# Performance work log

Measured on AMD Instinct MI355X. Metric: run time of the kernel, lower is better.

## Reference

```python
import jax, jax.numpy as jnp
import numpy as np

N_TOKENS = 2048
HIDDEN = 1024
INTER = 2816
N_EXPERTS = 8
N_ADAPTERS = 2
MAX_RANK = 16
TOP_K = 2
N_SEQS = 8


def setup_inputs() -> dict:
    key = jax.random.key(0)
    ks = jax.random.split(key, 12)
    f32 = jnp.float32
    std = 0.02
    hidden_states = jax.random.normal(ks[0], (N_TOKENS, HIDDEN), f32)
    topk_ids = jax.random.randint(ks[1], (N_TOKENS, TOP_K), 0, N_EXPERTS)
    tw = jax.random.uniform(ks[2], (N_TOKENS, TOP_K), dtype=f32)
    topk_weights = tw / tw.sum(axis=-1, keepdims=True)
    gate_a = jax.random.normal(ks[3], (N_ADAPTERS, N_EXPERTS, MAX_RANK, HIDDEN), f32) * std
    gate_b = jax.random.normal(ks[4], (N_ADAPTERS, N_EXPERTS, INTER, MAX_RANK), f32) * std
    up_a = jax.random.normal(ks[5], (N_ADAPTERS, N_EXPERTS, MAX_RANK, HIDDEN), f32) * std
    up_b = jax.random.normal(ks[6], (N_ADAPTERS, N_EXPERTS, INTER, MAX_RANK), f32) * std
    down_a = jax.random.normal(ks[7], (N_ADAPTERS, N_EXPERTS, MAX_RANK, INTER), f32) * std
    down_b = jax.random.normal(ks[8], (N_ADAPTERS, N_EXPERTS, HIDDEN, MAX_RANK), f32) * std
    weight_indices = jax.random.randint(ks[9], (N_SEQS,), 0, N_ADAPTERS)
    seq_lens = jnp.full((N_SEQS,), N_TOKENS // N_SEQS, dtype=jnp.int32)
    lora_ranks = jnp.array([16, 8], dtype=jnp.int32)
    scalings = jnp.array([2.0, 1.0], dtype=f32)
    base_gate_up_weight = jax.random.normal(ks[10], (N_EXPERTS, 2 * INTER, HIDDEN), f32) * std
    base_down_weight = jax.random.normal(ks[11], (N_EXPERTS, HIDDEN, INTER), f32) * std
    return {
        'hidden_states': hidden_states, 'topk_ids': topk_ids, 'topk_weights': topk_weights,
        'gate_a': gate_a, 'gate_b': gate_b, 'up_a': up_a, 'up_b': up_b,
        'down_a': down_a, 'down_b': down_b, 'weight_indices': weight_indices,
        'seq_lens': seq_lens, 'lora_ranks': lora_ranks, 'scalings': scalings,
        'base_gate_up_weight': base_gate_up_weight, 'base_down_weight': base_down_weight,
    }


def _forward(hidden_states, topk_ids, topk_weights, gate_a, gate_b, up_a, up_b,
             down_a, down_b, weight_indices, seq_lens, lora_ranks, scalings,
             base_gate_up_weight, base_down_weight):
    N, H = hidden_states.shape
    A, E, R, _ = gate_a.shape
    I = gate_b.shape[2]
    x = hidden_states.astype(jnp.float32)
    # token -> sequence -> adapter (replaces the per-token python loop)
    token_to_seq = jnp.searchsorted(jnp.cumsum(seq_lens), jnp.arange(N), side='right')
    adapter = weight_indices[token_to_seq]                               # [N]
    scale_t = scalings[adapter].astype(jnp.float32)[:, None]             # [N,1]
    # per-adapter rank truncation A[:rank] == zeroing rows r >= rank of LoRA-A
    rmask = (jnp.arange(R)[None, :] < lora_ranks[:, None]).astype(jnp.float32)  # [A,R]
    ga = gate_a.astype(jnp.float32) * rmask[:, None, :, None]
    ua = up_a.astype(jnp.float32) * rmask[:, None, :, None]
    da = down_a.astype(jnp.float32) * rmask[:, None, :, None]
    gb = gate_b.astype(jnp.float32)
    ub = up_b.astype(jnp.float32)
    db = down_b.astype(jnp.float32)
    # low-rank input projections for all adapters & experts (tiny: N*A*E*R)
    z_gate = jnp.einsum('nh,aerh->naer', x, ga)
    z_up = jnp.einsum('nh,aerh->naer', x, ua)
    sel = adapter[:, None, None]
    Wgu = base_gate_up_weight.astype(jnp.float32)   # [E, 2I, H]
    Wd = base_down_weight.astype(jnp.float32)       # [E, H, I]
    out = jnp.zeros((N, H), jnp.float32)
    for e in range(E):
        # summed routing weight for this expert per token (0 => no contribution)
        w_e = jnp.where(topk_ids == e, topk_weights, 0.0).sum(axis=1).astype(jnp.float32)  # [N]
        base_gate = x @ Wgu[e, :I].T                 # [N,I]
        base_up = x @ Wgu[e, I:].T                   # [N,I]
        lg = jnp.take_along_axis(jnp.einsum('nar,air->nai', z_gate[:, :, e], gb[:, e]), sel, axis=1)[:, 0]
        lu = jnp.take_along_axis(jnp.einsum('nar,air->nai', z_up[:, :, e], ub[:, e]), sel, axis=1)[:, 0]
        gate_out = base_gate + scale_t * lg
        up_out = base_up + scale_t * lu
        act = jax.nn.silu(gate_out) * up_out         # [N,I]
        zd = jnp.einsum('ni,ari->nar', act, da[:, e])
        ld = jnp.take_along_axis(jnp.einsum('nar,ahr->nah', zd, db[:, e]), sel, axis=1)[:, 0]
        base_down = act @ Wd[e].T                    # [N,H]
        out = out + w_e[:, None] * (base_down + scale_t * ld)
    return out.astype(hidden_states.dtype)


def reference(hidden_states, topk_ids, topk_weights, gate_a, gate_b, up_a, up_b,
              down_a, down_b, weight_indices, seq_lens, lora_ranks, scalings,
              base_gate_up_weight, base_down_weight):
    return _forward(hidden_states, topk_ids, topk_weights, gate_a, gate_b, up_a, up_b,
                    down_a, down_b, weight_indices, seq_lens, lora_ranks, scalings,
                    base_gate_up_weight, base_down_weight)
```

## Files before the change

### kernel.cpp

```cpp
#include <hip/hip_runtime.h>
#include <hip/hip_bf16.h>
#include <math.h>

#define N_TOK   2048
#define HIDDEN  1024
#define INTER   2816
#define NEXP    8
#define NADAPT  2
#define MAXRANK 16
#define TOPK    2
#define NSEQ    8
#define NPAIRS  (N_TOK*TOPK)
#define NGU     (2*INTER)

typedef unsigned short u16;
typedef __attribute__((ext_vector_type(8))) short bf16x8;
typedef __attribute__((ext_vector_type(4))) float f32x4;

#define F_CNT   0u
#define F_PERM  4096u
#define F_ZG    139264u
#define F_ZU    401408u
#define F_ZD    663552u
#define F_XBF   1048576u
#define F_ACT   5242880u
#define F_GB    28311552u
#define F_UB    29753344u
#define F_DB    31195136u
#define F_GA_BF 31719424u
#define F_UA_BF 32243712u
#define F_ZDF   32768000u
#define F_WGU   33554432u
#define F_WD    125829120u
#define F_DA_BF F_XBF
#define FAST_NEED 171966464u

#define B_CNT   0u
#define B_PERM  4096u
#define B_ZG    262144u
#define B_ZU    524288u
#define B_ZD    786432u
#define B_ACT   1048576u

__device__ __forceinline__ float bf2f(u16 u){
  union { unsigned int i; float f; } v; v.i = ((unsigned int)u)<<16; return v.f;
}
__device__ __forceinline__ u16 f2bf(float f){
  union { float f; unsigned int i; } v; v.f = f;
  unsigned int i = v.i;
  return (u16)((i + 0x7fffu + ((i>>16)&1u)) >> 16);
}
__device__ __forceinline__ uint4 cvt8(const float* src){
  float4 lo = *(const float4*)src;
  float4 hi = *(const float4*)(src+4);
  uint4 r;
  r.x = (unsigned)f2bf(lo.x) | ((unsigned)f2bf(lo.y)<<16);
  r.y = (unsigned)f2bf(lo.z) | ((unsigned)f2bf(lo.w)<<16);
  r.z = (unsigned)f2bf(hi.x) | ((unsigned)f2bf(hi.y)<<16);
  r.w = (unsigned)f2bf(hi.z) | ((unsigned)f2bf(hi.w)<<16);
  return r;
}
__device__ __forceinline__ uint2 cvt4(float4 v){
  uint2 r;
  r.x = (unsigned)f2bf(v.x) | ((unsigned)f2bf(v.y)<<16);
  r.y = (unsigned)f2bf(v.z) | ((unsigned)f2bf(v.w)<<16);
  return r;
}

__device__ __forceinline__ void gl16(const void* g, void* l){
  __builtin_amdgcn_global_load_lds(
      (const __attribute__((address_space(1))) unsigned int*)g,
      (__attribute__((address_space(3))) unsigned int*)l, 16, 0, 0);
}

__device__ __forceinline__ int token_adapter(int n, const int* seq_lens, const int* widx){
  int cum = 0;
  #pragma unroll
  for (int s = 0; s < NSEQ; ++s){ cum += seq_lens[s]; if (n < cum) return widx[s]; }
  return widx[NSEQ-1];
}

__global__ void k_zero(float* outf, int* cnt, float* zdf){
  int t = threadIdx.x;
  if (blockIdx.x < 2048){
    int id = blockIdx.x*256 + t;
    *(float4*)&outf[(size_t)id*4] = make_float4(0.f,0.f,0.f,0.f);
  } else {
    int id = (blockIdx.x - 2048)*256 + t;
    *(float4*)&zdf[(size_t)id*4] = make_float4(0.f,0.f,0.f,0.f);
  }
  if (blockIdx.x == 0 && t < NEXP) cnt[t] = 0;
}

__global__ void k_route(const int* __restrict__ topk_ids, int* cnt, int* perm){
  int p = blockIdx.x*256 + threadIdx.x;
  if (p >= NPAIRS) return;
  int e = topk_ids[p];
  int pos = atomicAdd(&cnt[e], 1);
  perm[e*NPAIRS + pos] = p;
}

__global__ void k_cvt(const float* __restrict__ src, u16* __restrict__ dst, int n4){
  int id = blockIdx.x*256 + threadIdx.x;
  if (id >= n4) return;
  ((uint2*)dst)[id] = cvt4(((const float4*)src)[id]);
}

__global__ void k_cvt_all(
    const float* __restrict__ x,  const float* __restrict__ wgu, const float* __restrict__ wd,
    const float* __restrict__ gb, const float* __restrict__ ub,  const float* __restrict__ db_,
    const float* __restrict__ ga, const float* __restrict__ ua,
    u16* xb, u16* wgub, u16* wdb, u16* gbb, u16* ubb, u16* dbb, u16* gab, u16* uab,
    float* outf, float* zdf, int* cnt)
{
  int b = blockIdx.x;
  int t = threadIdx.x;
  if (b == 0 && t < NEXP) cnt[t] = 0;
  if (b >= 35904){
    float* dz; size_t i4;
    if (b < 37952){ dz = outf; i4 = (size_t)(b - 35904)*256 + t; }
    else          { dz = zdf;  i4 = (size_t)(b - 37952)*256 + t; }
    ((float4*)dz)[i4] = make_float4(0.f,0.f,0.f,0.f);
    return;
  }
  const float* src; u16* dst; int base;
  if      (b < 1024)  { src = x;   dst = xb;   base = 0; }
  else if (b < 23552) { src = wgu; dst = wgub; base = 1024; }
  else if (b < 34816) { src = wd;  dst = wdb;  base = 23552; }
  else if (b < 35168) { src = gb;  dst = gbb;  base = 34816; }
  else if (b < 35520) { src = ub;  dst = ubb;  base = 35168; }
  else if (b < 35648) { src = db_; dst = dbb;  base = 35520; }
  else if (b < 35776) { src = ga;  dst = gab;  base = 35648; }
  else                { src = ua;  dst = uab;  base = 35776; }
  size_t i4 = (size_t)(b - base)*512 + t;
  float4 v0 = ((const float4*)src)[i4];
  float4 v1 = ((const float4*)src)[i4 + 256];
  ((uint2*)dst)[i4]       = cvt4(v0);
  ((uint2*)dst)[i4 + 256] = cvt4(v1);
}

__global__ __launch_bounds__(256) void k_zgu_mfma(
    const u16* __restrict__ xb, const u16* __restrict__ gab, const u16* __restrict__ uab,
    const int* __restrict__ cnt, const int* __restrict__ perm,
    const int* __restrict__ widx, const int* __restrict__ seq_lens,
    const int* __restrict__ ranks, const float* __restrict__ scal,
    u16* __restrict__ zg, u16* __restrict__ zu)
{
  int e = blockIdx.y;
  int me = cnt[e];
  int tm = blockIdx.x;
  if (tm*64 >= me) return;
  int t = threadIdx.x;

  __shared__ __align__(16) u16 As[64*32];
  __shared__ __align__(16) u16 Bs[64*32];

  int r0 = t >> 2;
  int kc = ((t&3) - r0) & 3;
  int ko = kc*8;
  int mg = tm*64 + r0;
  int pa = perm[e*NPAIRS + min(mg, me-1)];
  const u16* arow = xb + (size_t)(pa>>1)*HIDDEN + ko;
  int jr = r0 & 31;
  const u16* brow = (r0 < 32 ? gab : uab)
                    + (size_t)(((jr>>4)*NEXP + e)*MAXRANK + (jr&15))*HIDDEN + ko;

  int wv = t>>6, lane = t&63;
  u16* Asw = &As[wv*512];
  u16* Bsw = &Bs[wv*512];
  int wm = wv>>1, wn = wv&1;
  int l15 = lane&15, q = lane>>4;

  f32x4 acc[2][2] = {};
  int aoff[2], boff[2];
  #pragma unroll
  for (int i=0;i<2;++i){ int row = wm*32 + i*16 + l15; aoff[i] = row*32 + ((q+row)&3)*8; }
  #pragma unroll
  for (int j=0;j<2;++j){ int row = wn*32 + j*16 + l15; boff[j] = row*32 + ((q+row)&3)*8; }

  for (int kt = 0; kt < HIDDEN/32; ++kt){
    __syncthreads();
    gl16(arow + kt*32, Asw);
    gl16(brow + kt*32, Bsw);
    __syncthreads();
    bf16x8 af[2], bfr[2];
    #pragma unroll
    for (int i=0;i<2;++i) af[i] = *(const bf16x8*)&As[aoff[i]];
    #pragma unroll
    for (int j=0;j<2;++j) bfr[j] = *(const bf16x8*)&Bs[boff[j]];
    #pragma unroll
    for (int i=0;i<2;++i)
      #pragma unroll
      for (int j=0;j<2;++j)
        acc[i][j] = __builtin_amdgcn_mfma_f32_16x16x32_bf16(af[i], bfr[j], acc[i][j],0,0,0);
  }

  u16* dstz = wn ? zu : zg;
  #pragma unroll
  for (int i=0;i<2;++i){
    #pragma unroll
    for (int r=0;r<4;++r){
      int mgo = tm*64 + wm*32 + i*16 + q*4 + r;
      if (mgo < me){
        int p = perm[e*NPAIRS + mgo];
        int a = token_adapter(p>>1, seq_lens, widx);
        int rank = ranks[a]; float sc = scal[a];
        #pragma unroll
        for (int j=0;j<2;++j){
          int jc = j*16 + l15;
          float v = ((jc>>4)==a && (jc&15)<rank) ? sc*acc[i][j][r] : 0.f;
          dstz[(size_t)p*32 + jc] = f2bf(v);
        }
      }
    }
  }
}

__global__ __launch_bounds__(256) void k_zd_mfma(
    const u16* __restrict__ act, const u16* __restrict__ dab,
    const int* __restrict__ cnt, const int* __restrict__ perm,
    const int* __restrict__ widx, const int* __restrict__ seq_lens,
    const int* __restrict__ ranks, const float* __restrict__ scal,
    float* __restrict__ zdf)
{
  int e = blockIdx.z;
  int me = cnt[e];
  int tm = blockIdx.y;
  if (tm*64 >= me) return;
  int ks = blockIdx.x;
  int t = threadIdx.x;

  __shared__ __align__(16) u16 As[64*32];
  __shared__ __align__(16) u16 Bs[32*32];

  int r0 = t >> 2;
  int kc = ((t&3) - r0) & 3;
  int ko = kc*8;
  int mg = tm*64 + r0;
  int pa = perm[e*NPAIRS + min(mg, me-1)];
  const u16* arow = act + (size_t)pa*INTER + ko;
  int jr = r0 & 31;
  const u16* brow = dab + (size_t)(((jr>>4)*NEXP + e)*MAXRANK + (jr&15))*INTER + ko;

  int wv = t>>6, lane = t&63;
  u16* Asw = &As[wv*512];
  u16* Bsw = &Bs[(wv&1)*512];
  int l15 = lane&15, q = lane>>4;

  f32x4 acc[2] = {};
  int aoff; { int row = wv*16 + l15; aoff = row*32 + ((q+row)&3)*8; }
  int boff[2];
  #pragma unroll
  for (int j=0;j<2;++j){ int row = j*16 + l15; boff[j] = row*32 + ((q+row)&3)*8; }

  int kt0 = ks*22, kt1 = kt0 + 22;
  for (int kt = kt0; kt < kt1; ++kt){
    __syncthreads();
    gl16(arow + kt*32, Asw);
    if (wv < 2) gl16(brow + kt*32, Bsw);
    __syncthreads();
    bf16x8 af = *(const bf16x8*)&As[aoff];
    bf16x8 b0 = *(const bf16x8*)&Bs[boff[0]];
    bf16x8 b1 = *(const bf16x8*)&Bs[boff[1]];
    acc[0] = __builtin_amdgcn_mfma_f32_16x16x32_bf16(af, b0, acc[0],0,0,0);
    acc[1] = __builtin_amdgcn_mfma_f32_16x16x32_bf16(af, b1, acc[1],0,0,0);
  }

  #pragma unroll
  for (int r=0;r<4;++r){
    int mgo = tm*64 + wv*16 + q*4 + r;
    if (mgo < me){
      int p = perm[e*NPAIRS + mgo];
      int a = token_adapter(p>>1, seq_lens, widx);
      int rank = ranks[a]; float sc = scal[a];
      #pragma unroll
      for (int j=0;j<2;++j){
        int jc = j*16 + l15;
        if ((jc>>4)==a && (jc&15)<rank)
          atomicAdd(&zdf[(size_t)p*32 + jc], sc*acc[j][r]);
      }
    }
  }
}

__global__ __launch_bounds__(256) void k_zgu(
    const float* __restrict__ x, const int* __restrict__ topk_ids,
    const float* __restrict__ gate_a, const float* __restrict__ up_a,
    const int* __restrict__ widx, const int* __restrict__ seq_lens,
    const int* __restrict__ ranks, const float* __restrict__ scal,
    u16* __restrict__ zg, u16* __restrict__ zu)
{
  int p = blockIdx.x, n = p >> 1, t = threadIdx.x;
  int e = topk_ids[p];
  __shared__ float xs[HIDDEN];
  for (int i = t; i < HIDDEN; i += 256) xs[i] = x[(size_t)n*HIDDEN + i];
  if (t < 32){ zg[p*32 + t] = 0; zu[p*32 + t] = 0; }
  __syncthreads();
  int a = token_adapter(n, seq_lens, widx);
  int rank = ranks[a];
  float scale = scal[a];
  int wv = t >> 6, lane = t & 63;
  for (int i = 0; i < 8; ++i){
    int o = wv*8 + i;
    int r = o & 15;
    const float* wrow = ((o < 16) ? gate_a : up_a) + (size_t)((a*NEXP + e)*MAXRANK + r)*HIDDEN;
    float s = 0.f;
    for (int h = lane; h < HIDDEN; h += 64) s += xs[h] * wrow[h];
    s += __shfl_down(s,32); s += __shfl_down(s,16); s += __shfl_down(s,8);
    s += __shfl_down(s,4);  s += __shfl_down(s,2);  s += __shfl_down(s,1);
    if (lane == 0 && r < rank)
      (o < 16 ? zg : zu)[p*32 + a*16 + r] = f2bf(scale * s);
  }
}

__global__ __launch_bounds__(256) void k_zd(
    const u16* __restrict__ act, const int* __restrict__ topk_ids,
    const float* __restrict__ down_a,
    const int* __restrict__ widx, const int* __restrict__ seq_lens,
    const int* __restrict__ ranks, const float* __restrict__ scal,
    u16* __restrict__ zd)
{
  int p = blockIdx.x, n = p >> 1, t = threadIdx.x;
  int e = topk_ids[p];
  __shared__ float as_[INTER];
  for (int i = t; i < INTER; i += 256) as_[i] = bf2f(act[(size_t)p*INTER + i]);
  if (t < 32) zd[p*32 + t] = 0;
  __syncthreads();
  int a = token_adapter(n, seq_lens, widx);
  int rank = ranks[a];
  float scale = scal[a];
  int wv = t >> 6, lane = t & 63;
  for (int i = 0; i < 4; ++i){
    int r = wv*4 + i;
    const float* wrow = down_a + (size_t)((a*NEXP + e)*MAXRANK + r)*INTER;
    float s = 0.f;
    for (int h = lane; h < INTER; h += 64) s += as_[h] * wrow[h];
    s += __shfl_down(s,32); s += __shfl_down(s,16); s += __shfl_down(s,8);
    s += __shfl_down(s,4);  s += __shfl_down(s,2);  s += __shfl_down(s,1);
    if (lane == 0 && r < rank) zd[p*32 + a*16 + r] = f2bf(scale * s);
  }
}

__global__ __launch_bounds__(256) void k_gufused_bf(
    const u16* __restrict__ xb, const u16* __restrict__ wgu,
    const u16* __restrict__ gbb, const u16* __restrict__ ubb,
    const u16* __restrict__ zg, const u16* __restrict__ zu,
    const int* __restrict__ cnt, const int* __restrict__ perm,
    u16* __restrict__ act)
{
  int e = blockIdx.z;
  int me = cnt[e];
  int tm = blockIdx.y;
  if (tm*128 >= me) return;
  int tn = blockIdx.x;
  int t = threadIdx.x;

  __shared__ __align__(16) u16 As[128*32];
  __shared__ __align__(16) u16 Bg[64*32];
  __shared__ __align__(16) u16 Bu[64*32];

  int r0 = t >> 2;
  int kc = ((t&3) - r0) & 3;
  int ko = kc*8;
  int mg0 = tm*128 + r0, mg1 = mg0 + 64;
  int p0 = perm[e*NPAIRS + min(mg0, me-1)];
  int p1 = perm[e*NPAIRS + min(mg1, me-1)];
  const u16* arow0 = xb + (size_t)(p0>>1)*HIDDEN + ko;
  const u16* arow1 = xb + (size_t)(p1>>1)*HIDDEN + ko;
  int jg = tn*64 + r0;
  const u16* browg = wgu + ((size_t)e*NGU + jg)*HIDDEN + ko;
  const u16* browu = wgu + ((size_t)e*NGU + INTER + jg)*HIDDEN + ko;

  int wvb = (t>>6)*512;
  u16* Asw0 = &As[wvb];
  u16* Asw1 = &As[2048 + wvb];
  u16* Bgw  = &Bg[wvb];
  u16* Buw  = &Bu[wvb];

  int wv = t>>6, lane = t&63;
  int wm = wv>>1, wn = wv&1;
  int l15 = lane&15, q = lane>>4;

  f32x4 accg[4][2] = {};
  f32x4 accu[4][2] = {};
  int aoff[4], boff[2];
  #pragma unroll
  for (int i=0;i<4;++i){ int row = wm*64 + i*16 + l15; aoff[i] = row*32 + ((q+row)&3)*8; }
  #pragma unroll
  for (int j=0;j<2;++j){ int row = wn*32 + j*16 + l15; boff[j] = row*32 + ((q+row)&3)*8; }

  for (int kt = 0; kt < HIDDEN/32; ++kt){
    __syncthreads();
    gl16(arow0 + kt*32, Asw0);
    gl16(arow1 + kt*32, Asw1);
    gl16(browg + kt*32, Bgw);
    gl16(browu + kt*32, Buw);
    __syncthreads();
    bf16x8 af[4], bgf[2], buf[2];
    #pragma unroll
    for (int i=0;i<4;++i) af[i] = *(const bf16x8*)&As[aoff[i]];
    #pragma unroll
    for (int j=0;j<2;++j){ bgf[j] = *(const bf16x8*)&Bg[boff[j]]; buf[j] = *(const bf16x8*)&Bu[boff[j]]; }
    #pragma unroll
    for (int i=0;i<4;++i)
      #pragma unroll
      for (int j=0;j<2;++j){
        accg[i][j] = __builtin_amdgcn_mfma_f32_16x16x32_bf16(af[i], bgf[j], accg[i][j],0,0,0);
        accu[i][j] = __builtin_amdgcn_mfma_f32_16x16x32_bf16(af[i], buf[j], accu[i][j],0,0,0);
      }
  }
  {
    int aid = kc>>1, rr = (kc&1)*8;
    const u16* gB = gbb + ((size_t)(aid*NEXP+e)*INTER + jg)*MAXRANK + rr;
    const u16* uB = ubb + ((size_t)(aid*NEXP+e)*INTER + jg)*MAXRANK + rr;
    __syncthreads();
    gl16(zg + (size_t)p0*32 + ko, Asw0);
    gl16(zg + (size_t)p1*32 + ko, Asw1);
    gl16(gB, Bgw);
    __syncthreads();
    {
      bf16x8 af[4], bgf[2];
      #pragma unroll
      for (int i=0;i<4;++i) af[i] = *(const bf16x8*)&As[aoff[i]];
      #pragma unroll
      for (int j=0;j<2;++j) bgf[j] = *(const bf16x8*)&Bg[boff[j]];
      #pragma unroll
      for (int i=0;i<4;++i)
        #pragma unroll
        for (int j=0;j<2;++j)
          accg[i][j] = __builtin_amdgcn_mfma_f32_16x16x32_bf16(af[i], bgf[j], accg[i][j],0,0,0);
    }
    __syncthreads();
    gl16(zu + (size_t)p0*32 + ko, Asw0);
    gl16(zu + (size_t)p1*32 + ko, Asw1);
    gl16(uB, Bgw);
    __syncthreads();
    {
      bf16x8 af[4], buf[2];
      #pragma unroll
      for (int i=0;i<4;++i) af[i] = *(const bf16x8*)&As[aoff[i]];
      #pragma unroll
      for (int j=0;j<2;++j) buf[j] = *(const bf16x8*)&Bg[boff[j]];
      #pragma unroll
      for (int i=0;i<4;++i)
        #pragma unroll
        for (int j=0;j<2;++j)
          accu[i][j] = __builtin_amdgcn_mfma_f32_16x16x32_bf16(af[i], buf[j], accu[i][j],0,0,0);
    }
  }

  int col = l15, quad = q;
  #pragma unroll
  for (int i = 0; i < 4; ++i){
    #pragma unroll
    for (int r = 0; r < 4; ++r){
      int mg = tm*128 + wm*64 + i*16 + quad*4 + r;
      if (mg < me){
        int p = perm[e*NPAIRS + mg];
        size_t base = (size_t)p*INTER;
        #pragma unroll
        for (int j = 0; j < 2; ++j){
          int jc = tn*64 + wn*32 + j*16 + col;
          float g = accg[i][j][r], u = accu[i][j][r];
          float s = g / (1.f + __expf(-g));
          act[base + jc] = f2bf(s*u);
        }
      }
    }
  }
}

__global__ __launch_bounds__(256) void k_down_bf(
    const u16* __restrict__ act, const u16* __restrict__ wdb,
    const u16* __restrict__ dbb, const u16* __restrict__ zd,
    const float* __restrict__ tw,
    const int* __restrict__ cnt, const int* __restrict__ perm,
    float* __restrict__ outf)
{
  int e = blockIdx.z;
  int me = cnt[e];
  int tm = blockIdx.y;
  if (tm*128 >= me) return;
  int tn = blockIdx.x & 7;
  int ks = blockIdx.x >> 3;
  int t = threadIdx.x;

  __shared__ __align__(16) u16 As[128*32];
  __shared__ __align__(16) u16 Bs[128*32];

  int r0 = t >> 2;
  int kc = ((t&3) - r0) & 3;
  int ko = kc*8;
  int mg0 = tm*128 + r0, mg1 = mg0 + 64;
  int p0 = perm[e*NPAIRS + min(mg0, me-1)];
  int p1 = perm[e*NPAIRS + min(mg1, me-1)];
  const u16* arow0 = act + (size_t)p0*INTER + ko;
  const u16* arow1 = act + (size_t)p1*INTER + ko;
  int j0 = tn*128 + r0, j1 = j0 + 64;
  const u16* brow0 = wdb + ((size_t)e*HIDDEN + j0)*INTER + ko;
  const u16* brow1 = wdb + ((size_t)e*HIDDEN + j1)*INTER + ko;

  int wvb = (t>>6)*512;
  u16* Asw0 = &As[wvb];
  u16* Asw1 = &As[2048 + wvb];
  u16* Bsw0 = &Bs[wvb];
  u16* Bsw1 = &Bs[2048 + wvb];

  int wv = t>>6, lane = t&63;
  int wm = wv>>1, wn = wv&1;
  int l15 = lane&15, q = lane>>4;

  f32x4 acc[4][4] = {};
  int aoff[4], boff[4];
  #pragma unroll
  for (int i=0;i<4;++i){ int row = wm*64 + i*16 + l15; aoff[i] = row*32 + ((q+row)&3)*8; }
  #pragma unroll
  for (int j=0;j<4;++j){ int row = wn*64 + j*16 + l15; boff[j] = row*32 + ((q+row)&3)*8; }

  auto mma = [&](){
    bf16x8 af[4], bfr[4];
    #pragma unroll
    for (int i=0;i<4;++i){ af[i] = *(const bf16x8*)&As[aoff[i]]; bfr[i] = *(const bf16x8*)&Bs[boff[i]]; }
    #pragma unroll
    for (int i=0;i<4;++i)
      #pragma unroll
      for (int j=0;j<4;++j)
        acc[i][j] = __builtin_amdgcn_mfma_f32_16x16x32_bf16(af[i], bfr[j], acc[i][j],0,0,0);
  };

  int kt0 = ks*22, kt1 = kt0 + 22;
  for (int kt = kt0; kt < kt1; ++kt){
    __syncthreads();
    gl16(arow0 + kt*32, Asw0);
    gl16(arow1 + kt*32, Asw1);
    gl16(brow0 + kt*32, Bsw0);
    gl16(brow1 + kt*32, Bsw1);
    __syncthreads();
    mma();
  }
  if (ks == 3){
    int aid = kc>>1, rr = (kc&1)*8;
    __syncthreads();
    gl16(zd + (size_t)p0*32 + ko, Asw0);
    gl16(zd + (size_t)p1*32 + ko, Asw1);
    gl16(dbb + ((size_t)(aid*NEXP+e)*HIDDEN + j0)*MAXRANK + rr, Bsw0);
    gl16(dbb + ((size_t)(aid*NEXP+e)*HIDDEN + j1)*MAXRANK + rr, Bsw1);
    __syncthreads();
    mma();
  }

  int col = l15, quad = q;
  #pragma unroll
  for (int i = 0; i < 4; ++i){
    #pragma unroll
    for (int r = 0; r < 4; ++r){
      int mg = tm*128 + wm*64 + i*16 + quad*4 + r;
      if (mg < me){
        int p = perm[e*NPAIRS + mg];
        float wp = tw[p];
        size_t base = (size_t)(p >> 1)*HIDDEN;
        #pragma unroll
        for (int j = 0; j < 4; ++j){
          int jc = tn*128 + wn*64 + j*16 + col;
          atomicAdd(&outf[base + jc], wp * acc[i][j][r]);
        }
      }
    }
  }
}

__global__ __launch_bounds__(256) void k_gufused(
    const float* __restrict__ x, const float* __restrict__ wgu,
    const float* __restrict__ gate_b, const float* __restrict__ up_b,
    const u16* __restrict__ zg, const u16* __restrict__ zu,
    const int* __restrict__ cnt, const int* __restrict__ perm,
    u16* __restrict__ act)
{
  int e = blockIdx.z;
  int me = cnt[e];
  int tm = blockIdx.y;
  if (tm*128 >= me) return;
  int tn = blockIdx.x;
  int t = threadIdx.x;

  __shared__ __align__(16) u16 As[128*32];
  __shared__ __align__(16) u16 Bg[64*32];
  __shared__ __align__(16) u16 Bu[64*32];

  int r0 = t >> 2, cc = t & 3;
  int mg0 = tm*128 + r0, mg1 = mg0 + 64;
  int p0 = perm[e*NPAIRS + min(mg0, me-1)];
  int p1 = perm[e*NPAIRS + min(mg1, me-1)];
  const float* arow0 = x + (size_t)(p0 >> 1)*HIDDEN;
  const float* arow1 = x + (size_t)(p1 >> 1)*HIDDEN;
  int jg = tn*64 + r0;
  const float* browg = wgu + ((size_t)e*NGU + jg)*HIDDEN;
  const float* browu = wgu + ((size_t)e*NGU + INTER + jg)*HIDDEN;

  int wv = t >> 6, lane = t & 63;
  int wm = wv >> 1, wn = wv & 1;

  f32x4 accg[4][2] = {};
  f32x4 accu[4][2] = {};
  int aoff[4], boff[2];
  #pragma unroll
  for (int i = 0; i < 4; ++i) aoff[i] = (wm*64 + i*16 + (lane&15))*32 + (lane>>4)*8;
  #pragma unroll
  for (int j = 0; j < 2; ++j) boff[j] = (wn*32 + j*16 + (lane&15))*32 + (lane>>4)*8;

  for (int kt = 0; kt < HIDDEN/32; ++kt){
    uint4 a0 = cvt8(arow0 + kt*32 + cc*8);
    uint4 a1 = cvt8(arow1 + kt*32 + cc*8);
    uint4 bg = cvt8(browg + kt*32 + cc*8);
    uint4 bu = cvt8(browu + kt*32 + cc*8);
    __syncthreads();
    *(uint4*)&As[r0*32 + cc*8]      = a0;
    *(uint4*)&As[(r0+64)*32 + cc*8] = a1;
    *(uint4*)&Bg[r0*32 + cc*8]      = bg;
    *(uint4*)&Bu[r0*32 + cc*8]      = bu;
    __syncthreads();
    bf16x8 af[4], bgf[2], buf[2];
    #pragma unroll
    for (int i = 0; i < 4; ++i) af[i] = *(const bf16x8*)&As[aoff[i]];
    #pragma unroll
    for (int j = 0; j < 2; ++j){ bgf[j] = *(const bf16x8*)&Bg[boff[j]]; buf[j] = *(const bf16x8*)&Bu[boff[j]]; }
    #pragma unroll
    for (int i = 0; i < 4; ++i)
      #pragma unroll
      for (int j = 0; j < 2; ++j){
        accg[i][j] = __builtin_amdgcn_mfma_f32_16x16x32_bf16(af[i], bgf[j], accg[i][j], 0, 0, 0);
        accu[i][j] = __builtin_amdgcn_mfma_f32_16x16x32_bf16(af[i], buf[j], accu[i][j], 0, 0, 0);
      }
  }
  {
    uint4 a0 = *(const uint4*)(zg + (size_t)p0*32 + cc*8);
    uint4 a1 = *(const uint4*)(zg + (size_t)p1*32 + cc*8);
    int aid = cc >> 1, rr = (cc & 1)*8;
    uint4 bg = cvt8(gate_b + ((size_t)(aid*NEXP + e)*INTER + jg)*MAXRANK + rr);
    __syncthreads();
    *(uint4*)&As[r0*32 + cc*8]      = a0;
    *(uint4*)&As[(r0+64)*32 + cc*8] = a1;
    *(uint4*)&Bg[r0*32 + cc*8]      = bg;
    __syncthreads();
    bf16x8 af[4], bgf[2];
    #pragma unroll
    for (int i = 0; i < 4; ++i) af[i] = *(const bf16x8*)&As[aoff[i]];
    #pragma unroll
    for (int j = 0; j < 2; ++j) bgf[j] = *(const bf16x8*)&Bg[boff[j]];
    #pragma unroll
    for (int i = 0; i < 4; ++i)
      #pragma unroll
      for (int j = 0; j < 2; ++j)
        accg[i][j] = __builtin_amdgcn_mfma_f32_16x16x32_bf16(af[i], bgf[j], accg[i][j], 0, 0, 0);
  }
  {
    uint4 a0 = *(const uint4*)(zu + (size_t)p0*32 + cc*8);
    uint4 a1 = *(const uint4*)(zu + (size_t)p1*32 + cc*8);
    int aid = cc >> 1, rr = (cc & 1)*8;
    uint4 bu = cvt8(up_b + ((size_t)(aid*NEXP + e)*INTER + jg)*MAXRANK + rr);
    __syncthreads();
    *(uint4*)&As[r0*32 + cc*8]      = a0;
    *(uint4*)&As[(r0+64)*32 + cc*8] = a1;
    *(uint4*)&Bg[r0*32 + cc*8]      = bu;
    __syncthreads();
    bf16x8 af[4], buf[2];
    #pragma unroll
    for (int i = 0; i < 4; ++i) af[i] = *(const bf16x8*)&As[aoff[i]];
    #pragma unroll
    for (int j = 0; j < 2; ++j) buf[j] = *(const bf16x8*)&Bg[boff[j]];
    #pragma unroll
    for (int i = 0; i < 4; ++i)
      #pragma unroll
      for (int j = 0; j < 2; ++j)
        accu[i][j] = __builtin_amdgcn_mfma_f32_16x16x32_bf16(af[i], buf[j], accu[i][j], 0, 0, 0);
  }
  int col = lane & 15, quad = lane >> 4;
  #pragma unroll
  for (int i = 0; i < 4; ++i){
    #pragma unroll
    for (int r = 0; r < 4; ++r){
      int mg = tm*128 + wm*64 + i*16 + quad*4 + r;
      if (mg < me){
        int p = perm[e*NPAIRS + mg];
        size_t base = (size_t)p*INTER;
        #pragma unroll
        for (int j = 0; j < 2; ++j){
          int jc = tn*64 + wn*32 + j*16 + col;
          float g = accg[i][j][r], u = accu[i][j][r];
          float s = g / (1.f + __expf(-g));
          act[base + jc] = f2bf(s*u);
        }
      }
    }
  }
}

__global__ __launch_bounds__(256) void k_gemm_down(
    const u16* __restrict__ act, const float* __restrict__ wd,
    const float* __restrict__ down_b, const u16* __restrict__ zd,
    const float* __restrict__ tw,
    const int* __restrict__ cnt, const int* __restrict__ perm,
    float* __restrict__ outf)
{
  int e = blockIdx.z;
  int me = cnt[e];
  int tm = blockIdx.y;
  if (tm*128 >= me) return;
  int tn = blockIdx.x;
  int t = threadIdx.x;

  __shared__ __align__(16) u16 As[128*32];
  __shared__ __align__(16) u16 Bs[128*32];

  int r0 = t >> 2, cc = t & 3;
  int mg0 = tm*128 + r0, mg1 = mg0 + 64;
  int p0 = perm[e*NPAIRS + min(mg0, me-1)];
  int p1 = perm[e*NPAIRS + min(mg1, me-1)];
  const u16* arow0 = act + (size_t)p0*INTER;
  const u16* arow1 = act + (size_t)p1*INTER;
  int j0 = tn*128 + r0, j1 = j0 + 64;
  const float* brow0 = wd + ((size_t)e*HIDDEN + j0)*INTER;
  const float* brow1 = wd + ((size_t)e*HIDDEN + j1)*INTER;

  int wv = t >> 6, lane = t & 63;
  int wm = wv >> 1, wn = wv & 1;

  f32x4 acc[4][4] = {};
  int aoff[4], boff[4];
  #pragma unroll
  for (int i = 0; i < 4; ++i){
    aoff[i] = (wm*64 + i*16 + (lane&15))*32 + (lane>>4)*8;
    boff[i] = (wn*64 + i*16 + (lane&15))*32 + (lane>>4)*8;
  }

  auto compute = [&](){
    bf16x8 af[4], bfr[4];
    #pragma unroll
    for (int i = 0; i < 4; ++i){
      af[i]  = *(const bf16x8*)&As[aoff[i]];
      bfr[i] = *(const bf16x8*)&Bs[boff[i]];
    }
    #pragma unroll
    for (int i = 0; i < 4; ++i)
      #pragma unroll
      for (int j = 0; j < 4; ++j)
        acc[i][j] = __builtin_amdgcn_mfma_f32_16x16x32_bf16(af[i], bfr[j], acc[i][j], 0, 0, 0);
  };

  for (int kt = 0; kt < INTER/32; ++kt){
    uint4 a0 = *(const uint4*)(arow0 + kt*32 + cc*8);
    uint4 a1 = *(const uint4*)(arow1 + kt*32 + cc*8);
    uint4 b0 = cvt8(brow0 + kt*32 + cc*8);
    uint4 b1 = cvt8(brow1 + kt*32 + cc*8);
    __syncthreads();
    *(uint4*)&As[r0*32 + cc*8]      = a0;
    *(uint4*)&As[(r0+64)*32 + cc*8] = a1;
    *(uint4*)&Bs[r0*32 + cc*8]      = b0;
    *(uint4*)&Bs[(r0+64)*32 + cc*8] = b1;
    __syncthreads();
    compute();
  }
  {
    uint4 a0 = *(const uint4*)(zd + (size_t)p0*32 + cc*8);
    uint4 a1 = *(const uint4*)(zd + (size_t)p1*32 + cc*8);
    int aid = cc >> 1, rr = (cc & 1)*8;
    uint4 b0 = cvt8(down_b + ((size_t)(aid*NEXP + e)*HIDDEN + j0)*MAXRANK + rr);
    uint4 b1 = cvt8(down_b + ((size_t)(aid*NEXP + e)*HIDDEN + j1)*MAXRANK + rr);
    __syncthreads();
    *(uint4*)&As[r0*32 + cc*8]      = a0;
    *(uint4*)&As[(r0+64)*32 + cc*8] = a1;
    *(uint4*)&Bs[r0*32 + cc*8]      = b0;
    *(uint4*)&Bs[(r0+64)*32 + cc*8] = b1;
    __syncthreads();
    compute();
  }
  int col = lane & 15, quad = lane >> 4;
  #pragma unroll
  for (int i = 0; i < 4; ++i){
    #pragma unroll
    for (int r = 0; r < 4; ++r){
      int mg = tm*128 + wm*64 + i*16 + quad*4 + r;
      if (mg < me){
        int p = perm[e*NPAIRS + mg];
        float wp = tw[p];
        size_t base = (size_t)(p >> 1)*HIDDEN;
        #pragma unroll
        for (int j = 0; j < 4; ++j){
          int jc = tn*128 + wn*64 + j*16 + col;
          atomicAdd(&outf[base + jc], wp * acc[i][j][r]);
        }
      }
    }
  }
}

extern "C" void kernel_launch(void* const* d_in, const int* in_sizes, int n_in,
                              void* d_out, int out_size, void* d_ws, size_t ws_size,
                              hipStream_t stream){
  const float* x        = (const float*)d_in[0];
  const int*   topk_ids = (const int*)d_in[1];
  const float* tw       = (const float*)d_in[2];
  const float* gate_a   = (const float*)d_in[3];
  const float* gate_b   = (const float*)d_in[4];
  const float* up_a     = (const float*)d_in[5];
  const float* up_b     = (const float*)d_in[6];
  const float* down_a   = (const float*)d_in[7];
  const float* down_b   = (const float*)d_in[8];
  const int*   widx     = (const int*)d_in[9];
  const int*   seq_lens = (const int*)d_in[10];
  const int*   ranks    = (const int*)d_in[11];
  const float* scal     = (const float*)d_in[12];
  const float* wgu      = (const float*)d_in[13];
  const float* wd       = (const float*)d_in[14];
  float* outf = (float*)d_out;
  char* ws = (char*)d_ws;

  if (ws_size >= (size_t)FAST_NEED){
    int* cnt  = (int*)(ws + F_CNT);
    int* perm = (int*)(ws + F_PERM);
    u16* zg   = (u16*)(ws + F_ZG);
    u16* zu   = (u16*)(ws + F_ZU);
    u16* zd   = (u16*)(ws + F_ZD);
    u16* xb   = (u16*)(ws + F_XBF);
    u16* act  = (u16*)(ws + F_ACT);
    u16* gbb  = (u16*)(ws + F_GB);
    u16* ubb  = (u16*)(ws + F_UB);
    u16* dbb  = (u16*)(ws + F_DB);
    u16* gab  = (u16*)(ws + F_GA_BF);
    u16* uab  = (u16*)(ws + F_UA_BF);
    float* zdf= (float*)(ws + F_ZDF);
    u16* dab  = (u16*)(ws + F_DA_BF);
    u16* wgub = (u16*)(ws + F_WGU);
    u16* wdb  = (u16*)(ws + F_WD);

    hipLaunchKernelGGL(k_cvt_all, dim3(38080), dim3(256), 0, stream,
                       x, wgu, wd, gate_b, up_b, down_b, gate_a, up_a,
                       xb, wgub, wdb, gbb, ubb, dbb, gab, uab,
                       outf, zdf, cnt);
    hipLaunchKernelGGL(k_route, dim3(16), dim3(256), 0, stream, topk_ids, cnt, perm);
    hipLaunchKernelGGL(k_zgu_mfma, dim3(64, NEXP), dim3(256), 0, stream,
                       xb, gab, uab, cnt, perm, widx, seq_lens, ranks, scal, zg, zu);
    hipLaunchKernelGGL(k_gufused_bf, dim3(INTER/64, 32, NEXP), dim3(256), 0, stream,
                       xb, wgub, gbb, ubb, zg, zu, cnt, perm, act);
    hipLaunchKernelGGL(k_cvt, dim3((NADAPT*NEXP*MAXRANK*INTER/4+255)/256), dim3(256), 0, stream,
                       down_a, dab, NADAPT*NEXP*MAXRANK*INTER/4);
    hipLaunchKernelGGL(k_zd_mfma, dim3(4, 64, NEXP), dim3(256), 0, stream,
                       act, dab, cnt, perm, widx, seq_lens, ranks, scal, zdf);
    hipLaunchKernelGGL(k_cvt, dim3((NPAIRS*32/4+255)/256), dim3(256), 0, stream,
                       zdf, zd, NPAIRS*32/4);
    hipLaunchKernelGGL(k_down_bf, dim3(32, 32, NEXP), dim3(256), 0, stream,
                       act, wdb, dbb, zd, tw, cnt, perm, outf);
  } else {
    int* cnt  = (int*)(ws + B_CNT);
    int* perm = (int*)(ws + B_PERM);
    u16* zg   = (u16*)(ws + B_ZG);
    u16* zu   = (u16*)(ws + B_ZU);
    u16* zd   = (u16*)(ws + B_ZD);
    u16* act  = (u16*)(ws + B_ACT);

    hipLaunchKernelGGL(k_zero,  dim3(2048), dim3(256), 0, stream, outf, cnt, outf);
    hipLaunchKernelGGL(k_route, dim3(16), dim3(256), 0, stream, topk_ids, cnt, perm);
    hipLaunchKernelGGL(k_zgu,   dim3(NPAIRS), dim3(256), 0, stream,
                       x, topk_ids, gate_a, up_a, widx, seq_lens, ranks, scal, zg, zu);
    hipLaunchKernelGGL(k_gufused, dim3(INTER/64, 32, NEXP), dim3(256), 0, stream,
                       x, wgu, gate_b, up_b, zg, zu, cnt, perm, act);
    hipLaunchKernelGGL(k_zd,    dim3(NPAIRS), dim3(256), 0, stream,
                       act, topk_ids, down_a, widx, seq_lens, ranks, scal, zd);
    hipLaunchKernelGGL(k_gemm_down, dim3(HIDDEN/128, 32, NEXP), dim3(256), 0, stream,
                       act, wd, down_b, zd, tw, cnt, perm, outf);
  }
}
```

Measured before the change: 620.1 us.

## Overlap bf16 weight conversion with the LoRA-A and gate/up GEMM kernels

```diff
diff --git a/kernel.cpp b/kernel.cpp
--- a/kernel.cpp
+++ b/kernel.cpp
@@ -67,6 +67,32 @@
   return r;
 }
 
+__device__ __forceinline__ void cvt_chunk8k(const float* __restrict__ src, u16* __restrict__ dst, int c, int t){
+  size_t b4 = (size_t)c*2048 + t;
+  float4 v0 = ((const float4*)src)[b4];
+  float4 v1 = ((const float4*)src)[b4 + 256];
+  float4 v2 = ((const float4*)src)[b4 + 512];
+  float4 v3 = ((const float4*)src)[b4 + 768];
+  float4 v4 = ((const float4*)src)[b4 + 1024];
+  float4 v5 = ((const float4*)src)[b4 + 1280];
+  float4 v6 = ((const float4*)src)[b4 + 1536];
+  float4 v7 = ((const float4*)src)[b4 + 1792];
+  ((uint2*)dst)[b4]        = cvt4(v0);
+  ((uint2*)dst)[b4 + 256]  = cvt4(v1);
+  ((uint2*)dst)[b4 + 512]  = cvt4(v2);
+  ((uint2*)dst)[b4 + 768]  = cvt4(v3);
+  ((uint2*)dst)[b4 + 1024] = cvt4(v4);
+  ((uint2*)dst)[b4 + 1280] = cvt4(v5);
+  ((uint2*)dst)[b4 + 1536] = cvt4(v6);
+  ((uint2*)dst)[b4 + 1792] = cvt4(v7);
+}
+__device__ __forceinline__ void zero_chunk8k(float* dst, int c, int t){
+  size_t b4 = (size_t)c*2048 + t;
+  #pragma unroll
+  for (int i = 0; i < 8; ++i)
+    ((float4*)dst)[b4 + i*256] = make_float4(0.f,0.f,0.f,0.f);
+}
+
 __device__ __forceinline__ void gl16(const void* g, void* l){
   __builtin_amdgcn_global_load_lds(
       (const __attribute__((address_space(1))) unsigned int*)g,
@@ -106,51 +132,42 @@
   ((uint2*)dst)[id] = cvt4(((const float4*)src)[id]);
 }
 
-__global__ void k_cvt_all(
-    const float* __restrict__ x,  const float* __restrict__ wgu, const float* __restrict__ wd,
-    const float* __restrict__ gb, const float* __restrict__ ub,  const float* __restrict__ db_,
-    const float* __restrict__ ga, const float* __restrict__ ua,
-    u16* xb, u16* wgub, u16* wdb, u16* gbb, u16* ubb, u16* dbb, u16* gab, u16* uab,
+__global__ void k_prep(
+    const float* __restrict__ x,  const float* __restrict__ gb, const float* __restrict__ ub,
+    const float* __restrict__ ga, const float* __restrict__ ua, const float* __restrict__ db_,
+    u16* xb, u16* gbb, u16* ubb, u16* gab, u16* uab, u16* dbb,
     float* outf, float* zdf, int* cnt)
 {
-  int b = blockIdx.x;
-  int t = threadIdx.x;
+  int b = blockIdx.x, t = threadIdx.x;
   if (b == 0 && t < NEXP) cnt[t] = 0;
-  if (b >= 35904){
-    float* dz; size_t i4;
-    if (b < 37952){ dz = outf; i4 = (size_t)(b - 35904)*256 + t; }
-    else          { dz = zdf;  i4 = (size_t)(b - 37952)*256 + t; }
-    ((float4*)dz)[i4] = make_float4(0.f,0.f,0.f,0.f);
-    return;
-  }
-  const float* src; u16* dst; int base;
-  if      (b < 1024)  { src = x;   dst = xb;   base = 0; }
-  else if (b < 23552) { src = wgu; dst = wgub; base = 1024; }
-  else if (b < 34816) { src = wd;  dst = wdb;  base = 23552; }
-  else if (b < 35168) { src = gb;  dst = gbb;  base = 34816; }
-  else if (b < 35520) { src = ub;  dst = ubb;  base = 35168; }
-  else if (b < 35648) { src = db_; dst = dbb;  base = 35520; }
-  else if (b < 35776) { src = ga;  dst = gab;  base = 35648; }
-  else                { src = ua;  dst = uab;  base = 35776; }
-  size_t i4 = (size_t)(b - base)*512 + t;
-  float4 v0 = ((const float4*)src)[i4];
-  float4 v1 = ((const float4*)src)[i4 + 256];
-  ((uint2*)dst)[i4]       = cvt4(v0);
-  ((uint2*)dst)[i4 + 256] = cvt4(v1);
-}
-
-__global__ __launch_bounds__(256) void k_zgu_mfma(
+  if      (b < 256) cvt_chunk8k(x,   xb,  b,       t);
+  else if (b < 344) cvt_chunk8k(gb,  gbb, b - 256, t);
+  else if (b < 432) cvt_chunk8k(ub,  ubb, b - 344, t);
+  else if (b < 464) cvt_chunk8k(ga,  gab, b - 432, t);
+  else if (b < 496) cvt_chunk8k(ua,  uab, b - 464, t);
+  else if (b < 528) cvt_chunk8k(db_, dbb, b - 496, t);
+  else if (b < 784) zero_chunk8k(outf, b - 528, t);
+  else              zero_chunk8k(zdf,  b - 784, t);
+}
+
+__global__ __launch_bounds__(256) void k_zgu_plus(
     const u16* __restrict__ xb, const u16* __restrict__ gab, const u16* __restrict__ uab,
+    const float* __restrict__ wgu_f32, u16* __restrict__ wgub,
     const int* __restrict__ cnt, const int* __restrict__ perm,
     const int* __restrict__ widx, const int* __restrict__ seq_lens,
     const int* __restrict__ ranks, const float* __restrict__ scal,
     u16* __restrict__ zg, u16* __restrict__ zu)
 {
+  int bx = blockIdx.x, t = threadIdx.x;
+  if (bx >= 64){
+    int c = blockIdx.y*704 + (bx - 64);
+    cvt_chunk8k(wgu_f32, wgub, c, t);
+    return;
+  }
   int e = blockIdx.y;
   int me = cnt[e];
-  int tm = blockIdx.x;
+  int tm = bx;
   if (tm*64 >= me) return;
-  int t = threadIdx.x;
 
   __shared__ __align__(16) u16 As[64*32];
   __shared__ __align__(16) u16 Bs[64*32];
@@ -341,19 +358,25 @@
   }
 }
 
-__global__ __launch_bounds__(256) void k_gufused_bf(
+__global__ __launch_bounds__(256) void k_gufused_plus(
     const u16* __restrict__ xb, const u16* __restrict__ wgu,
     const u16* __restrict__ gbb, const u16* __restrict__ ubb,
     const u16* __restrict__ zg, const u16* __restrict__ zu,
+    const float* __restrict__ wd_f32, u16* __restrict__ wdb_out,
     const int* __restrict__ cnt, const int* __restrict__ perm,
     u16* __restrict__ act)
 {
+  int tn = blockIdx.x;
+  int t = threadIdx.x;
+  if (tn >= 44){
+    int c = (tn - 44)*256 + (blockIdx.z*32 + blockIdx.y);
+    if (c < 2816) cvt_chunk8k(wd_f32, wdb_out, c, t);
+    return;
+  }
   int e = blockIdx.z;
   int me = cnt[e];
   int tm = blockIdx.y;
   if (tm*128 >= me) return;
-  int tn = blockIdx.x;
-  int t = threadIdx.x;
 
   __shared__ __align__(16) u16 As[128*32];
   __shared__ __align__(16) u16 Bg[64*32];
@@ -833,15 +856,14 @@
     u16* wgub = (u16*)(ws + F_WGU);
     u16* wdb  = (u16*)(ws + F_WD);
 
-    hipLaunchKernelGGL(k_cvt_all, dim3(38080), dim3(256), 0, stream,
-                       x, wgu, wd, gate_b, up_b, down_b, gate_a, up_a,
-                       xb, wgub, wdb, gbb, ubb, dbb, gab, uab,
-                       outf, zdf, cnt);
+    hipLaunchKernelGGL(k_prep, dim3(800), dim3(256), 0, stream,
+                       x, gate_b, up_b, gate_a, up_a, down_b,
+                       xb, gbb, ubb, gab, uab, dbb, outf, zdf, cnt);
     hipLaunchKernelGGL(k_route, dim3(16), dim3(256), 0, stream, topk_ids, cnt, perm);
-    hipLaunchKernelGGL(k_zgu_mfma, dim3(64, NEXP), dim3(256), 0, stream,
-                       xb, gab, uab, cnt, perm, widx, seq_lens, ranks, scal, zg, zu);
-    hipLaunchKernelGGL(k_gufused_bf, dim3(INTER/64, 32, NEXP), dim3(256), 0, stream,
-                       xb, wgub, gbb, ubb, zg, zu, cnt, perm, act);
+    hipLaunchKernelGGL(k_zgu_plus, dim3(64 + 704, NEXP), dim3(256), 0, stream,
+                       xb, gab, uab, wgu, wgub, cnt, perm, widx, seq_lens, ranks, scal, zg, zu);
+    hipLaunchKernelGGL(k_gufused_plus, dim3(44 + 11, 32, NEXP), dim3(256), 0, stream,
+                       xb, wgub, gbb, ubb, zg, zu, wd, wdb, cnt, perm, act);
     hipLaunchKernelGGL(k_cvt, dim3((NADAPT*NEXP*MAXRANK*INTER/4+255)/256), dim3(256), 0, stream,
                        down_a, dab, NADAPT*NEXP*MAXRANK*INTER/4);
     hipLaunchKernelGGL(k_zd_mfma, dim3(4, 64, NEXP), dim3(256), 0, stream,
```

New measurement: 621.8 us. Within noise of the previous version (+0.3%).
